# Kernel tuning notes

Hardware: AMD Instinct MI355X
Metric: run time of the kernel (lower is better)

## Reference

```python
import jax, jax.numpy as jnp
import numpy as np

B, L, F = 256, 512, 64
NUM_IDS = 2000
LN_EPS = 1e-5


def setup_inputs() -> dict:
    key = jax.random.key(0)
    ks = jax.random.split(key, 16)
    s = 0.05
    return {
        # padded neighbor-id sequences; 0 is the padding id
        "src_ids": jax.random.randint(ks[0], (B, L), 0, NUM_IDS, dtype=jnp.int64)
        if jax.config.jax_enable_x64 else jax.random.randint(ks[0], (B, L), 0, NUM_IDS, dtype=jnp.int32),
        "dst_ids": jax.random.randint(ks[1], (B, L), 0, NUM_IDS, dtype=jnp.int64)
        if jax.config.jax_enable_x64 else jax.random.randint(ks[1], (B, L), 0, NUM_IDS, dtype=jnp.int32),
        # co-occurrence encode MLP: Linear(1->F), ReLU, Linear(F->F)
        "enc_w1": jax.random.normal(ks[2], (1, F), jnp.float32) * s,
        "enc_b1": jax.random.normal(ks[3], (F,), jnp.float32) * s,
        "enc_w2": jax.random.normal(ks[4], (F, F), jnp.float32) * s,
        "enc_b2": jax.random.normal(ks[5], (F,), jnp.float32) * s,
        # cross-attention projections (bias-free q/k/v as in source)
        "Wq": jax.random.normal(ks[6], (F, F), jnp.float32) * s,
        "Wk": jax.random.normal(ks[7], (F, F), jnp.float32) * s,
        "Wv": jax.random.normal(ks[8], (F, F), jnp.float32) * s,
        "Wo": jax.random.normal(ks[9], (F, F), jnp.float32) * s,
        "bo": jax.random.normal(ks[10], (F,), jnp.float32) * s,
        "ln_g": jnp.ones((F,), jnp.float32),
        "ln_b": jnp.zeros((F,), jnp.float32),
    }


def _counts_in(a, b):
    # for each element of a: how many times does it occur in b (same batch row)
    # equivalent to the np.unique count / mapping-dict lookup in the original
    return (a[:, :, None] == b[:, None, :]).sum(axis=-1).astype(jnp.float32)


def _appearances(a, b):
    # [B, L, 2]: counts of each id of `a` in (a, b); zero out padding (id==0)
    app = jnp.stack([_counts_in(a, a), _counts_in(a, b)], axis=-1)
    return jnp.where((a == 0)[..., None], 0.0, app)


def _encode(app, w1, b1, w2, b2):
    # Linear(1->F) -> ReLU -> Linear(F->F), then sum over the 2 count channels
    h = jax.nn.relu(app[..., None] * w1[0] + b1)  # [B, L, 2, F]
    h = jnp.einsum('blcf,fg->blcg', h, w2) + b2
    return h.sum(axis=2)  # [B, L, F]


def _linear_attn(q, k, v):
    dim = q.shape[-1]
    q = jax.nn.softmax(q, axis=-1) * (dim ** -0.5)
    k = jax.nn.softmax(k, axis=1)  # softmax over sequence dim (dim=-2)
    ctx = jnp.einsum('bld,ble->bde', k, v)
    return jnp.einsum('bld,bde->ble', q, ctx)


def _layer_norm(x, g, b):
    mu = x.mean(axis=-1, keepdims=True)
    var = ((x - mu) ** 2).mean(axis=-1, keepdims=True)
    return (x - mu) * jax.lax.rsqrt(var + LN_EPS) * g + b


def _cross_attn(x, ctx, Wq, Wk, Wv, Wo, bo, ln_g, ln_b):
    q, k, v = x @ Wq, ctx @ Wk, ctx @ Wv
    attn = _linear_attn(q, k, v)
    return _layer_norm(x + attn @ Wo + bo, ln_g, ln_b)


def reference(src_ids, dst_ids, enc_w1, enc_b1, enc_w2, enc_b2,
              Wq, Wk, Wv, Wo, bo, ln_g, ln_b):
    # neighbor co-occurrence counting + encoding
    src_app = _appearances(src_ids, dst_ids)  # [B, L, 2]
    dst_app = _appearances(dst_ids, src_ids)
    src_feat = _encode(src_app, enc_w1, enc_b1, enc_w2, enc_b2)  # [B, L, F]
    dst_feat = _encode(dst_app, enc_w1, enc_b1, enc_w2, enc_b2)
    # linear cross-attention fusion (shared weights, both directions)
    src_out = _cross_attn(src_feat, dst_feat, Wq, Wk, Wv, Wo, bo, ln_g, ln_b)
    dst_out = _cross_attn(dst_feat, src_feat, Wq, Wk, Wv, Wo, bo, ln_g, ln_b)
    return jnp.stack([src_out, dst_out])  # [2, B, L, F]
```

## Files before the change

### kernel.cpp

```cpp
#include <hip/hip_runtime.h>
#include <hip/hip_bf16.h>

#define BB 256
#define LL 512

typedef float nfloat4 __attribute__((ext_vector_type(4)));

__global__ __launch_bounds__(256, 2) void k_all(
    const int* __restrict__ src, const int* __restrict__ dst,
    const float* __restrict__ w1, const float* __restrict__ b1,
    const float* __restrict__ w2, const float* __restrict__ b2,
    const float* __restrict__ Wq, const float* __restrict__ Wk,
    const float* __restrict__ Wv, const float* __restrict__ Wo,
    const float* __restrict__ bo, const float* __restrict__ lng,
    const float* __restrict__ lnb, float* __restrict__ out) {
  __shared__ __align__(16) char smem[77840];
  int*   hist  = (int*)smem;
  float* poolF = (float*)smem;
  int*   hkey  = (int*)(smem + 16384);
  int*   hmult = (int*)(smem + 20480);
  float* tabL  = (float*)(smem + 16384);
  int*   cflag = (int*)(smem + 49152);
  int*   clist = (int*)(smem + 51252);
  float* Mg    = (float*)(smem + 49152);
  int*   xkey  = (int*)(smem + 66560);
  int*   ckey  = (int*)(smem + 68608);
  int*   cmult = (int*)(smem + 70656);
  int*   pidxl = (int*)(smem + 72704);
  float* fbF   = (float*)(smem + 74752);
  int*   npp   = (int*)(smem + 77824);

  int bd = blockIdx.x, b = bd >> 1, dir = bd & 1;
  int tid = threadIdx.x, tx = tid & 63, ty = tid >> 6;
  int e0 = ty * 16;

  const int* s = src + b * LL;
  const int* d = dst + b * LL;
  int sid0 = s[tid], sid1 = s[tid + 256];
  int did0 = d[tid], did1 = d[tid + 256];
  for (int i = tid; i < 4000; i += 256) hist[i] = 0;
  __syncthreads();
  atomicAdd(&hist[sid0], 1);        atomicAdd(&hist[sid1], 1);
  atomicAdd(&hist[2000 + did0], 1); atomicAdd(&hist[2000 + did1], 1);
  __syncthreads();

  int x0 = dir ? did0 : sid0, x1 = dir ? did1 : sid1;
  int c0 = dir ? sid0 : did0, c1 = dir ? sid1 : did1;
  const int* hx = dir ? hist + 2000 : hist;
  const int* hc = dir ? hist : hist + 2000;

  for (int i = tid; i < 1024; i += 256) { hkey[i] = -1; hmult[i] = 0; }
  if (tid == 0) *npp = 0;
  __syncthreads();
  for (int r = 0; r < 2; ++r) {
    int id = r ? c1 : c0;
    int ca = 0, cb = 0;
    if (id != 0) { ca = hc[id]; cb = hx[id]; }
    int key = ca | (cb << 10);
    int h = (int)(((unsigned)key * 2654435761u) >> 22) & 1023;
    while (true) {
      int old = atomicCAS(&hkey[h], -1, key);
      if (old == -1 || old == key) break;
      h = (h + 1) & 1023;
    }
    atomicAdd(&hmult[h], 1);
  }
  __syncthreads();
  for (int i = tid; i < 1024; i += 256) {
    if (hkey[i] != -1) {
      int idx = atomicAdd(npp, 1);
      ckey[idx]  = hkey[i];
      cmult[idx] = hmult[i];
    }
  }
  __syncthreads();
  int Pc = *npp;
  __syncthreads();

  for (int i = tid; i < 1024; i += 256) { hkey[i] = -1; }
  if (tid == 0) *npp = 0;
  __syncthreads();
  int slot0, slot1;
  for (int r = 0; r < 2; ++r) {
    int id = r ? x1 : x0;
    int ca = 0, cb = 0;
    if (id != 0) { ca = hx[id]; cb = hc[id]; }
    int key = ca | (cb << 10);
    int h = (int)(((unsigned)key * 2654435761u) >> 22) & 1023;
    while (true) {
      int old = atomicCAS(&hkey[h], -1, key);
      if (old == -1 || old == key) break;
      h = (h + 1) & 1023;
    }
    if (r) slot1 = h; else slot0 = h;
  }
  __syncthreads();
  for (int i = tid; i < 1024; i += 256) {
    int k = hkey[i];
    if (k != -1) {
      int idx = atomicAdd(npp, 1);
      xkey[idx] = k;
      hkey[i] = idx;
    }
  }
  __syncthreads();
  pidxl[tid]       = hkey[slot0];
  pidxl[tid + 256] = hkey[slot1];
  int Px = *npp;
  __syncthreads();

  for (int i = tid; i < 513; i += 256) cflag[i] = 0;
  if (tid == 0) *npp = 0;
  __syncthreads();
  if (tid < Pc) { int k = ckey[tid]; cflag[k & 1023] = 1; cflag[k >> 10] = 1; }
  if (tid < Px) { int k = xkey[tid]; cflag[k & 1023] = 1; cflag[k >> 10] = 1; }
  __syncthreads();
  for (int c = tid; c < 513; c += 256) {
    if (cflag[c]) {
      int idx = atomicAdd(npp, 1);
      clist[idx] = c;
      cflag[c] = idx;
    }
  }
  __syncthreads();
  int nc = *npp;
  if (tid < Pc) { int k = ckey[tid]; ckey[tid] = cflag[k & 1023] | (cflag[k >> 10] << 10); }
  if (tid < Px) { int k = xkey[tid]; xkey[tid] = cflag[k & 1023] | (cflag[k >> 10] << 10); }
  __syncthreads();

  float wa[64];
#pragma unroll
  for (int f = 0; f < 64; ++f) wa[f] = w2[f * 64 + tx];
  {
    float w1v = w1[tx], b1v = b1[tx], b2v = b2[tx];
    for (int i = ty; i < nc; i += 4) {
      float c = (float)clist[i];
      poolF[ty * 64 + tx] = fmaxf(c * w1v + b1v, 0.f);
      float acc = b2v;
      const float4* h4 = (const float4*)&poolF[ty * 64];
#pragma unroll
      for (int q = 0; q < 16; ++q) {
        float4 hv = h4[q];
        acc += hv.x * wa[4 * q] + hv.y * wa[4 * q + 1] + hv.z * wa[4 * q + 2] + hv.w * wa[4 * q + 3];
      }
      tabL[i * 64 + tx] = acc;
    }
  }
  __syncthreads();

  float* featA = poolF;
  float* pA    = poolF + 1024;
  float* vA    = poolF + 2048;
  float macc[16];
#pragma unroll
  for (int e = 0; e < 16; ++e) macc[e] = 0.f;
  float sacc = 0.f;

  for (int j0 = 0; j0 < Pc; j0 += 16) {
    int cN = min(16, Pc - j0);
#pragma unroll
    for (int f = 0; f < 64; ++f) wa[f] = Wk[f * 64 + tx];
    for (int j = ty; j < cN; j += 4) {
      int key = ckey[j0 + j];
      int ia = key & 1023, ib = key >> 10;
      featA[j * 64 + tx] = tabL[ia * 64 + tx] + tabL[ib * 64 + tx];
      float kr = 0.f;
      const float4* fb4 = (const float4*)&featA[j * 64];
#pragma unroll
      for (int q = 0; q < 16; ++q) {
        float4 fv = fb4[q];
        kr += fv.x * wa[4 * q] + fv.y * wa[4 * q + 1] + fv.z * wa[4 * q + 2] + fv.w * wa[4 * q + 3];
      }
      float p = __expf(kr) * (float)cmult[j0 + j];
      sacc += p;
      pA[j * 64 + tx] = p;
    }
#pragma unroll
    for (int f = 0; f < 64; ++f) wa[f] = Wv[f * 64 + tx];
    for (int j = ty; j < cN; j += 4) {
      float vr = 0.f;
      const float4* fb4 = (const float4*)&featA[j * 64];
#pragma unroll
      for (int q = 0; q < 16; ++q) {
        float4 fv = fb4[q];
        vr += fv.x * wa[4 * q] + fv.y * wa[4 * q + 1] + fv.z * wa[4 * q + 2] + fv.w * wa[4 * q + 3];
      }
      vA[j * 64 + tx] = vr;
    }
    __syncthreads();
    for (int jj = 0; jj < cN; ++jj) {
      float pg = pA[jj * 64 + tx];
      const float4* vb4 = (const float4*)&vA[jj * 64 + e0];
#pragma unroll
      for (int q = 0; q < 4; ++q) {
        float4 vv = vb4[q];
        macc[4 * q]     += pg * vv.x; macc[4 * q + 1] += pg * vv.y;
        macc[4 * q + 2] += pg * vv.z; macc[4 * q + 3] += pg * vv.w;
      }
    }
    __syncthreads();
  }
  fbF[512 + ty * 64 + tx] = sacc;
  __syncthreads();
  float inv = 1.f / (fbF[512 + tx] + fbF[576 + tx] + fbF[640 + tx] + fbF[704 + tx]);
#pragma unroll
  for (int e = 0; e < 16; ++e) Mg[(e0 + e) * 68 + tx] = macc[e] * inv;
  for (int i = tid; i < 4096; i += 256) poolF[i] = Wo[i];
#pragma unroll
  for (int f = 0; f < 64; ++f) wa[f] = Wq[f * 64 + tx];
  float bov = bo[tx], lg = lng[tx], lb = lnb[tx];
  __syncthreads();

#pragma unroll
  for (int e = 0; e < 16; ++e) macc[e] = 0.f;
  for (int f = 0; f < 64; ++f) {
    float mt = Mg[f * 68 + tx];
    const float4* wo4 = (const float4*)&poolF[f * 64 + e0];
#pragma unroll
    for (int q = 0; q < 4; ++q) {
      float4 w4 = wo4[q];
      macc[4 * q]     += mt * w4.x; macc[4 * q + 1] += mt * w4.y;
      macc[4 * q + 2] += mt * w4.z; macc[4 * q + 3] += mt * w4.w;
    }
  }
  __syncthreads();
#pragma unroll
  for (int e = 0; e < 16; ++e) Mg[(e0 + e) * 68 + tx] = macc[e];
  __syncthreads();

  for (int i0 = 0; i0 < Px; i0 += 64) {
    int cN = min(64, Px - i0);
    for (int jj = ty; jj < cN; jj += 4) {
      int key = xkey[i0 + jj];
      int ia = key & 1023, ib = key >> 10;
      float fv = tabL[ia * 64 + tx] + tabL[ib * 64 + tx];
      fbF[ty * 64 + tx] = fv;
      float qr = 0.f;
      const float4* fb4 = (const float4*)&fbF[ty * 64];
#pragma unroll
      for (int q = 0; q < 16; ++q) {
        float4 f4v = fb4[q];
        qr += f4v.x * wa[4 * q] + f4v.y * wa[4 * q + 1] + f4v.z * wa[4 * q + 2] + f4v.w * wa[4 * q + 3];
      }
      float p = __expf(qr);
      float sum = p;
#pragma unroll
      for (int off = 32; off >= 1; off >>= 1) sum += __shfl_xor(sum, off, 64);
      float qh = p / sum * 0.125f;
      fbF[256 + ty * 64 + tx] = qh;
      float at = 0.f;
      const float4* qb4 = (const float4*)&fbF[256 + ty * 64];
      const float4* gt4 = (const float4*)&Mg[tx * 68];
#pragma unroll
      for (int q = 0; q < 16; ++q) {
        float4 qv = qb4[q];
        float4 gv = gt4[q];
        at += qv.x * gv.x + qv.y * gv.y + qv.z * gv.z + qv.w * gv.w;
      }
      float r = fv + at + bov;
      float mu = r;
#pragma unroll
      for (int off = 32; off >= 1; off >>= 1) mu += __shfl_xor(mu, off, 64);
      mu *= (1.f / 64.f);
      float dv = r - mu;
      float var = dv * dv;
#pragma unroll
      for (int off = 32; off >= 1; off >>= 1) var += __shfl_xor(var, off, 64);
      var *= (1.f / 64.f);
      poolF[jj * 64 + tx] = dv * rsqrtf(var + 1e-5f) * lg + lb;
    }
    __syncthreads();
    const nfloat4* w4 = (const nfloat4*)poolF;
    nfloat4* out4 = (nfloat4*)(out + (size_t)(dir * BB + b) * (LL * 64));
    for (int idx = tid; idx < 512 * 16; idx += 256) {
      int l = idx >> 4, q = idx & 15;
      int pid = pidxl[l];
      if (pid >= i0 && pid < i0 + cN)
        __builtin_nontemporal_store(w4[(pid - i0) * 16 + q], &out4[l * 16 + q]);
    }
    __syncthreads();
  }
}

extern "C" void kernel_launch(void* const* d_in, const int* in_sizes, int n_in,
                              void* d_out, int out_size, void* d_ws, size_t ws_size,
                              hipStream_t stream) {
  const int* src  = (const int*)d_in[0];
  const int* dst  = (const int*)d_in[1];
  const float* w1 = (const float*)d_in[2];
  const float* b1 = (const float*)d_in[3];
  const float* w2 = (const float*)d_in[4];
  const float* b2 = (const float*)d_in[5];
  const float* Wq = (const float*)d_in[6];
  const float* Wk = (const float*)d_in[7];
  const float* Wv = (const float*)d_in[8];
  const float* Wo = (const float*)d_in[9];
  const float* bo = (const float*)d_in[10];
  const float* lng = (const float*)d_in[11];
  const float* lnb = (const float*)d_in[12];
  float* out = (float*)d_out;

  k_all<<<dim3(512), dim3(256), 0, stream>>>(src, dst, w1, b1, w2, b2,
                                             Wq, Wk, Wv, Wo, bo, lng, lnb, out);
}
```

Before: 120.7 us.

## Merge dedup hash passes, fuse K/V projection, and shrink shared memory

Both the context and query co-occurrence keys now go through one shared hash table, with a side bit telling them apart, so several clear and compaction phases and their __syncthreads barriers go away. The K and V projections are computed in a single pass, keeping both weight matrices in registers (128 floats), over chunks of 32 rows instead of 16. The shared-memory layout is repacked down to about 63 KB, which could raise occupancy. The costs are higher register pressure, which may cause spills or lower occupancy, and more chance of collisions in the single combined hash table.

```diff
diff --git a/kernel.cpp b/kernel.cpp
--- a/kernel.cpp
+++ b/kernel.cpp
@@ -14,21 +14,21 @@
     const float* __restrict__ Wv, const float* __restrict__ Wo,
     const float* __restrict__ bo, const float* __restrict__ lng,
     const float* __restrict__ lnb, float* __restrict__ out) {
-  __shared__ __align__(16) char smem[77840];
+  __shared__ __align__(16) char smem[63776];
   int*   hist  = (int*)smem;
   float* poolF = (float*)smem;
   int*   hkey  = (int*)(smem + 16384);
   int*   hmult = (int*)(smem + 20480);
   float* tabL  = (float*)(smem + 16384);
-  int*   cflag = (int*)(smem + 49152);
-  int*   clist = (int*)(smem + 51252);
-  float* Mg    = (float*)(smem + 49152);
-  int*   xkey  = (int*)(smem + 66560);
-  int*   ckey  = (int*)(smem + 68608);
-  int*   cmult = (int*)(smem + 70656);
-  int*   pidxl = (int*)(smem + 72704);
-  float* fbF   = (float*)(smem + 74752);
-  int*   npp   = (int*)(smem + 77824);
+  float* Mg    = (float*)(smem + 32768);
+  int*   xkey  = (int*)(smem + 50176);
+  int*   ckey  = (int*)(smem + 52224);
+  int*   cmult = (int*)(smem + 54272);
+  int*   pidxl = (int*)(smem + 56320);
+  int*   cflag = (int*)(smem + 58368);
+  int*   clist = (int*)(smem + 60424);
+  float* fbF   = (float*)(smem + 60688);
+  int*   npp   = (int*)(smem + 63760);
 
   int bd = blockIdx.x, b = bd >> 1, dir = bd & 1;
   int tid = threadIdx.x, tx = tid & 63, ty = tid >> 6;
@@ -39,7 +39,11 @@
   int sid0 = s[tid], sid1 = s[tid + 256];
   int did0 = d[tid], did1 = d[tid + 256];
   for (int i = tid; i < 4000; i += 256) hist[i] = 0;
-  __syncthreads();
+  for (int i = tid; i < 1024; i += 256) { hkey[i] = -1; hmult[i] = 0; }
+  for (int i = tid; i < 513; i += 256) cflag[i] = 0;
+  if (tid < 3) npp[tid] = 0;
+  __syncthreads();
+
   atomicAdd(&hist[sid0], 1);        atomicAdd(&hist[sid1], 1);
   atomicAdd(&hist[2000 + did0], 1); atomicAdd(&hist[2000 + did1], 1);
   __syncthreads();
@@ -49,142 +53,107 @@
   const int* hx = dir ? hist + 2000 : hist;
   const int* hc = dir ? hist : hist + 2000;
 
-  for (int i = tid; i < 1024; i += 256) { hkey[i] = -1; hmult[i] = 0; }
-  if (tid == 0) *npp = 0;
-  __syncthreads();
-  for (int r = 0; r < 2; ++r) {
-    int id = r ? c1 : c0;
+  int slot0 = 0, slot1 = 0;
+#pragma unroll
+  for (int r = 0; r < 4; ++r) {
+    int side = r >> 1;
+    int id = (r == 0) ? c0 : (r == 1) ? c1 : (r == 2) ? x0 : x1;
     int ca = 0, cb = 0;
-    if (id != 0) { ca = hc[id]; cb = hx[id]; }
-    int key = ca | (cb << 10);
+    if (id != 0) {
+      if (side == 0) { ca = hc[id]; cb = hx[id]; }
+      else           { ca = hx[id]; cb = hc[id]; }
+    }
+    int key = ca | (cb << 10) | (side << 20);
     int h = (int)(((unsigned)key * 2654435761u) >> 22) & 1023;
     while (true) {
       int old = atomicCAS(&hkey[h], -1, key);
       if (old == -1 || old == key) break;
       h = (h + 1) & 1023;
     }
-    atomicAdd(&hmult[h], 1);
-  }
-  __syncthreads();
-  for (int i = tid; i < 1024; i += 256) {
-    if (hkey[i] != -1) {
-      int idx = atomicAdd(npp, 1);
-      ckey[idx]  = hkey[i];
-      cmult[idx] = hmult[i];
-    }
-  }
-  __syncthreads();
-  int Pc = *npp;
-  __syncthreads();
-
-  for (int i = tid; i < 1024; i += 256) { hkey[i] = -1; }
-  if (tid == 0) *npp = 0;
-  __syncthreads();
-  int slot0, slot1;
-  for (int r = 0; r < 2; ++r) {
-    int id = r ? x1 : x0;
-    int ca = 0, cb = 0;
-    if (id != 0) { ca = hx[id]; cb = hc[id]; }
-    int key = ca | (cb << 10);
-    int h = (int)(((unsigned)key * 2654435761u) >> 22) & 1023;
-    while (true) {
-      int old = atomicCAS(&hkey[h], -1, key);
-      if (old == -1 || old == key) break;
-      h = (h + 1) & 1023;
-    }
-    if (r) slot1 = h; else slot0 = h;
-  }
-  __syncthreads();
+    if (side == 0) atomicAdd(&hmult[h], 1);
+    else if (r == 2) slot0 = h;
+    else slot1 = h;
+  }
+  __syncthreads();
+
   for (int i = tid; i < 1024; i += 256) {
     int k = hkey[i];
     if (k != -1) {
-      int idx = atomicAdd(npp, 1);
-      xkey[idx] = k;
-      hkey[i] = idx;
-    }
-  }
-  __syncthreads();
+      if (k & (1 << 20)) {
+        int idx = atomicAdd(&npp[1], 1);
+        xkey[idx] = k & 0xFFFFF;
+        hkey[i] = idx;
+      } else {
+        int idx = atomicAdd(&npp[0], 1);
+        ckey[idx]  = k;
+        cmult[idx] = hmult[i];
+      }
+    }
+  }
+  __syncthreads();
+  int Pc = npp[0], Px = npp[1];
   pidxl[tid]       = hkey[slot0];
   pidxl[tid + 256] = hkey[slot1];
-  int Px = *npp;
-  __syncthreads();
-
-  for (int i = tid; i < 513; i += 256) cflag[i] = 0;
-  if (tid == 0) *npp = 0;
-  __syncthreads();
-  if (tid < Pc) { int k = ckey[tid]; cflag[k & 1023] = 1; cflag[k >> 10] = 1; }
-  if (tid < Px) { int k = xkey[tid]; cflag[k & 1023] = 1; cflag[k >> 10] = 1; }
+  for (int i = tid; i < Pc; i += 256) { int k = ckey[i]; cflag[k & 1023] = 1; cflag[k >> 10] = 1; }
+  for (int i = tid; i < Px; i += 256) { int k = xkey[i]; cflag[k & 1023] = 1; cflag[k >> 10] = 1; }
   __syncthreads();
   for (int c = tid; c < 513; c += 256) {
     if (cflag[c]) {
-      int idx = atomicAdd(npp, 1);
+      int idx = atomicAdd(&npp[2], 1);
       clist[idx] = c;
       cflag[c] = idx;
     }
   }
   __syncthreads();
-  int nc = *npp;
-  if (tid < Pc) { int k = ckey[tid]; ckey[tid] = cflag[k & 1023] | (cflag[k >> 10] << 10); }
-  if (tid < Px) { int k = xkey[tid]; xkey[tid] = cflag[k & 1023] | (cflag[k >> 10] << 10); }
-  __syncthreads();
-
-  float wa[64];
-#pragma unroll
-  for (int f = 0; f < 64; ++f) wa[f] = w2[f * 64 + tx];
+  int nc = npp[2];
+  for (int i = tid; i < Pc; i += 256) { int k = ckey[i]; ckey[i] = cflag[k & 1023] | (cflag[k >> 10] << 10); }
+  for (int i = tid; i < Px; i += 256) { int k = xkey[i]; xkey[i] = cflag[k & 1023] | (cflag[k >> 10] << 10); }
+
+  float wcA[64], wcB[64];
+#pragma unroll
+  for (int f = 0; f < 64; ++f) wcA[f] = w2[f * 64 + tx];
   {
     float w1v = w1[tx], b1v = b1[tx], b2v = b2[tx];
     for (int i = ty; i < nc; i += 4) {
       float c = (float)clist[i];
-      poolF[ty * 64 + tx] = fmaxf(c * w1v + b1v, 0.f);
+      fbF[ty * 64 + tx] = fmaxf(c * w1v + b1v, 0.f);
       float acc = b2v;
-      const float4* h4 = (const float4*)&poolF[ty * 64];
+      const float4* h4 = (const float4*)&fbF[ty * 64];
 #pragma unroll
       for (int q = 0; q < 16; ++q) {
         float4 hv = h4[q];
-        acc += hv.x * wa[4 * q] + hv.y * wa[4 * q + 1] + hv.z * wa[4 * q + 2] + hv.w * wa[4 * q + 3];
+        acc += hv.x * wcA[4 * q] + hv.y * wcA[4 * q + 1] + hv.z * wcA[4 * q + 2] + hv.w * wcA[4 * q + 3];
       }
       tabL[i * 64 + tx] = acc;
     }
   }
-  __syncthreads();
-
-  float* featA = poolF;
-  float* pA    = poolF + 1024;
-  float* vA    = poolF + 2048;
+#pragma unroll
+  for (int f = 0; f < 64; ++f) { wcA[f] = Wk[f * 64 + tx]; wcB[f] = Wv[f * 64 + tx]; }
   float macc[16];
 #pragma unroll
   for (int e = 0; e < 16; ++e) macc[e] = 0.f;
   float sacc = 0.f;
-
-  for (int j0 = 0; j0 < Pc; j0 += 16) {
-    int cN = min(16, Pc - j0);
-#pragma unroll
-    for (int f = 0; f < 64; ++f) wa[f] = Wk[f * 64 + tx];
+  __syncthreads();
+
+  float* pA = poolF;
+  float* vA = poolF + 2048;
+  for (int j0 = 0; j0 < Pc; j0 += 32) {
+    int cN = min(32, Pc - j0);
     for (int j = ty; j < cN; j += 4) {
       int key = ckey[j0 + j];
       int ia = key & 1023, ib = key >> 10;
-      featA[j * 64 + tx] = tabL[ia * 64 + tx] + tabL[ib * 64 + tx];
-      float kr = 0.f;
-      const float4* fb4 = (const float4*)&featA[j * 64];
+      fbF[ty * 64 + tx] = tabL[ia * 64 + tx] + tabL[ib * 64 + tx];
+      float kr = 0.f, vr = 0.f;
+      const float4* fb4 = (const float4*)&fbF[ty * 64];
 #pragma unroll
       for (int q = 0; q < 16; ++q) {
         float4 fv = fb4[q];
-        kr += fv.x * wa[4 * q] + fv.y * wa[4 * q + 1] + fv.z * wa[4 * q + 2] + fv.w * wa[4 * q + 3];
+        kr += fv.x * wcA[4 * q] + fv.y * wcA[4 * q + 1] + fv.z * wcA[4 * q + 2] + fv.w * wcA[4 * q + 3];
+        vr += fv.x * wcB[4 * q] + fv.y * wcB[4 * q + 1] + fv.z * wcB[4 * q + 2] + fv.w * wcB[4 * q + 3];
       }
       float p = __expf(kr) * (float)cmult[j0 + j];
       sacc += p;
       pA[j * 64 + tx] = p;
-    }
-#pragma unroll
-    for (int f = 0; f < 64; ++f) wa[f] = Wv[f * 64 + tx];
-    for (int j = ty; j < cN; j += 4) {
-      float vr = 0.f;
-      const float4* fb4 = (const float4*)&featA[j * 64];
-#pragma unroll
-      for (int q = 0; q < 16; ++q) {
-        float4 fv = fb4[q];
-        vr += fv.x * wa[4 * q] + fv.y * wa[4 * q + 1] + fv.z * wa[4 * q + 2] + fv.w * wa[4 * q + 3];
-      }
       vA[j * 64 + tx] = vr;
     }
     __syncthreads();
@@ -207,7 +176,7 @@
   for (int e = 0; e < 16; ++e) Mg[(e0 + e) * 68 + tx] = macc[e] * inv;
   for (int i = tid; i < 4096; i += 256) poolF[i] = Wo[i];
 #pragma unroll
-  for (int f = 0; f < 64; ++f) wa[f] = Wq[f * 64 + tx];
+  for (int f = 0; f < 64; ++f) wcA[f] = Wq[f * 64 + tx];
   float bov = bo[tx], lg = lng[tx], lb = lnb[tx];
   __syncthreads();
 
@@ -240,7 +209,7 @@
 #pragma unroll
       for (int q = 0; q < 16; ++q) {
         float4 f4v = fb4[q];
-        qr += f4v.x * wa[4 * q] + f4v.y * wa[4 * q + 1] + f4v.z * wa[4 * q + 2] + f4v.w * wa[4 * q + 3];
+        qr += f4v.x * wcA[4 * q] + f4v.y * wcA[4 * q + 1] + f4v.z * wcA[4 * q + 2] + f4v.w * wcA[4 * q + 3];
       }
       float p = __expf(qr);
       float sum = p;
```

Result: no change. 119.9 us (-0.7%).
